# Optimization experiments

Measured on AMD Instinct MI355X. Metric: run time of the kernel, lower is better.

The kernel has to match this reference:

```python
import jax, jax.numpy as jnp
import numpy as np
import math

B, T, H, NB, D = 4, 4096, 16, 32, 1024
HID = 128

def setup_inputs() -> dict:
    key = jax.random.key(0)
    ks = jax.random.split(key, 12)
    s = lambda k, shape, fan: jax.random.normal(k, shape, jnp.float32) * (1.0 / np.sqrt(fan))
    return {
        "theta_path": jax.random.normal(ks[0], (B, T, H, NB), jnp.float32),
        "content_emb": jax.random.normal(ks[1], (B, T, D), jnp.float32),
        "mw1": s(ks[2], (D, HID), D), "mb1": jnp.zeros((HID,), jnp.float32),
        "mw2": s(ks[3], (HID, H * NB), HID), "mb2": jnp.zeros((H * NB,), jnp.float32),
        "gw1": s(ks[4], (D, HID), D), "gb1": jnp.zeros((HID,), jnp.float32),
        "gw2": s(ks[5], (HID, H * NB), HID), "gb2": jnp.zeros((H * NB,), jnp.float32),
        "log_Q": jnp.full((H, NB), -3.0, jnp.float32),
        "log_R": jnp.full((H, NB), 1.0, jnp.float32),
        "log_sigma0": jnp.zeros((H, NB), jnp.float32),
    }

def reference(theta_path, content_emb, mw1, mb1, mw2, mb2, gw1, gb1, gw2, gb2, log_Q, log_R, log_sigma0):
    b, t = theta_path.shape[:2]
    Q = jnp.exp(log_Q)          # (H, NB)
    R = jnp.exp(log_R)          # (H, NB)
    sigma0 = jnp.exp(log_sigma0)
    # measurement head and gate (exact GELU as in torch nn.GELU default)
    h1 = jax.nn.gelu(content_emb @ mw1 + mb1, approximate=False)
    z = jnp.pi * jnp.tanh((h1 @ mw2 + mb2).reshape(b, t, H, NB))
    h2 = jax.nn.gelu(content_emb @ gw1 + gb1, approximate=False)
    g = jax.nn.sigmoid((h2 @ gw2 + gb2).reshape(b, t, H, NB))
    # per-step increments: incs[0]=theta_path[0], incs[t]=theta_path[t]-theta_path[t-1]
    incs = jnp.concatenate([theta_path[:, :1], theta_path[:, 1:] - theta_path[:, :-1]], axis=1)

    def step(carry, xs):
        theta_hat, sigma = carry
        inc_t, z_t, g_t = xs                     # each (B, H, NB)
        theta_hat = theta_hat + inc_t
        sigma = sigma + Q
        diff = z_t - theta_hat
        innov = jnp.arctan2(jnp.sin(diff), jnp.cos(diff))
        R_eff = R / (g_t + 1e-4)
        K = sigma / (sigma + R_eff)
        theta_hat = theta_hat + K * innov
        sigma = (1.0 - K) * sigma
        return (theta_hat, sigma), (theta_hat, sigma)

    init = (jnp.zeros((b, H, NB), theta_path.dtype),
            jnp.broadcast_to(sigma0, (b, H, NB)))
    xs = (jnp.swapaxes(incs, 0, 1), jnp.swapaxes(z, 0, 1), jnp.swapaxes(g, 0, 1))
    _, (theta_seq, sigma_seq) = jax.lax.scan(step, init, xs)
    theta_hat_out = jnp.swapaxes(theta_seq, 0, 1)   # (B, T, H, NB)
    sigma_out = jnp.swapaxes(sigma_seq, 0, 1)
    return theta_hat_out, sigma_out, g
```

## Files before the change

kernel.cpp:

```cpp
#include <hip/hip_runtime.h>
#include <cstdint>
#include <cstddef>

typedef _Float16 half8  __attribute__((ext_vector_type(8)));
typedef float    f32x4  __attribute__((ext_vector_type(4)));

constexpr int Bc = 4, Tc = 4096, Hc = 16, NBc = 32, Dc = 1024, HIDc = 128;
constexpr int HN = Hc * NBc;
constexpr int BT = Bc * Tc;

__device__ inline void split8(const float* __restrict__ p,
                              _Float16* __restrict__ dh,
                              _Float16* __restrict__ dl) {
  float4 a = *reinterpret_cast<const float4*>(p);
  float4 b = *reinterpret_cast<const float4*>(p + 4);
  float v[8] = {a.x, a.y, a.z, a.w, b.x, b.y, b.z, b.w};
  half8 hi, lo;
#pragma unroll
  for (int j = 0; j < 8; j++) {
    _Float16 h = (_Float16)v[j];
    hi[j] = h;
    lo[j] = (_Float16)(v[j] - (float)h);
  }
  *reinterpret_cast<half8*>(dh) = hi;
  *reinterpret_cast<half8*>(dl) = lo;
}

__global__ __launch_bounds__(256) void k_split_w(
    const float* __restrict__ mw1, const float* __restrict__ gw1,
    const float* __restrict__ mw2, const float* __restrict__ gw2,
    _Float16* __restrict__ W1Thi, _Float16* __restrict__ W1Tlo,
    _Float16* __restrict__ W2Thi, _Float16* __restrict__ W2Tlo) {
  unsigned i = blockIdx.x * 256u + threadIdx.x;
  if (i < 262144u) {
    unsigned n = i >> 10, k = i & 1023u;
    float v = (n < 128u) ? mw1[k * 128u + n] : gw1[k * 128u + (n - 128u)];
    _Float16 h = (_Float16)v;
    W1Thi[i] = h;
    W1Tlo[i] = (_Float16)(v - (float)h);
  } else {
    unsigned j2 = i - 262144u;
    unsigned n = j2 >> 7, k = j2 & 127u;
    float v = (n < 512u) ? mw2[k * 512u + n] : gw2[k * 512u + (n - 512u)];
    _Float16 h = (_Float16)v;
    W2Thi[j2] = h;
    W2Tlo[j2] = (_Float16)(v - (float)h);
  }
}

__global__ __launch_bounds__(256) void k_gemm1(
    const float* __restrict__ X,
    const _Float16* __restrict__ Whi, const _Float16* __restrict__ Wlo,
    const float* __restrict__ mb1, const float* __restrict__ gb1,
    _Float16* __restrict__ Hhi, _Float16* __restrict__ Hlo) {
  __shared__ _Float16 sAh[128][40], sAl[128][40];
  __shared__ _Float16 sBh[64][40],  sBl[64][40];
  const int tid  = threadIdx.x;
  const int lane = tid & 63;
  const int w    = tid >> 6;
  const int wr   = w >> 1, wc = w & 1;
  const int rm   = blockIdx.x * 128;
  const int cn   = blockIdx.y * 64;
  const int lr   = lane & 15, kg = (lane >> 4) * 8;

  f32x4 acc[4][2] = {};

  for (int kt = 0; kt < 1024; kt += 32) {
#pragma unroll
    for (int j = 0; j < 2; j++) {
      int row = j * 64 + (tid >> 2);
      int k0  = (tid & 3) * 8;
      size_t g = (size_t)(rm + row) * 1024 + kt + k0;
      split8(X + g, &sAh[row][k0], &sAl[row][k0]);
    }
    {
      int n  = tid >> 2;
      int k0 = (tid & 3) * 8;
      size_t g = (size_t)(cn + n) * 1024 + kt + k0;
      *reinterpret_cast<uint4*>(&sBh[n][k0]) = *reinterpret_cast<const uint4*>(Whi + g);
      *reinterpret_cast<uint4*>(&sBl[n][k0]) = *reinterpret_cast<const uint4*>(Wlo + g);
    }
    __syncthreads();

    half8 ah[4], al[4], bh[2], bl[2];
#pragma unroll
    for (int m = 0; m < 4; m++) {
      ah[m] = *reinterpret_cast<const half8*>(&sAh[wr * 64 + m * 16 + lr][kg]);
      al[m] = *reinterpret_cast<const half8*>(&sAl[wr * 64 + m * 16 + lr][kg]);
    }
#pragma unroll
    for (int n = 0; n < 2; n++) {
      bh[n] = *reinterpret_cast<const half8*>(&sBh[wc * 32 + n * 16 + lr][kg]);
      bl[n] = *reinterpret_cast<const half8*>(&sBl[wc * 32 + n * 16 + lr][kg]);
    }
#pragma unroll
    for (int m = 0; m < 4; m++)
#pragma unroll
      for (int n = 0; n < 2; n++) {
        acc[m][n] = __builtin_amdgcn_mfma_f32_16x16x32_f16(ah[m], bh[n], acc[m][n], 0, 0, 0);
        acc[m][n] = __builtin_amdgcn_mfma_f32_16x16x32_f16(ah[m], bl[n], acc[m][n], 0, 0, 0);
        acc[m][n] = __builtin_amdgcn_mfma_f32_16x16x32_f16(al[m], bh[n], acc[m][n], 0, 0, 0);
      }
    __syncthreads();
  }

#pragma unroll
  for (int n = 0; n < 2; n++) {
    int colg = cn + wc * 32 + n * 16 + lr;
    float bias = (colg < 128) ? mb1[colg] : gb1[colg - 128];
#pragma unroll
    for (int m = 0; m < 4; m++) {
#pragma unroll
      for (int r = 0; r < 4; r++) {
        int rowg = rm + wr * 64 + m * 16 + (lane >> 4) * 4 + r;
        float v  = acc[m][n][r] + bias;
        float ge = 0.5f * v * (1.0f + erff(v * 0.70710678118654752f));
        _Float16 h = (_Float16)ge;
        Hhi[(size_t)rowg * 256 + colg] = h;
        Hlo[(size_t)rowg * 256 + colg] = (_Float16)(ge - (float)h);
      }
    }
  }
}

__global__ __launch_bounds__(256) void k_gemm2(
    const _Float16* __restrict__ Hhi, const _Float16* __restrict__ Hlo,
    const _Float16* __restrict__ Whi, const _Float16* __restrict__ Wlo,
    const float* __restrict__ mb2, const float* __restrict__ gb2,
    float* __restrict__ zbuf, float* __restrict__ gout) {
  __shared__ _Float16 sAh[128][40], sAl[128][40];
  __shared__ _Float16 sBh[64][40],  sBl[64][40];
  const int tid  = threadIdx.x;
  const int lane = tid & 63;
  const int w    = tid >> 6;
  const int wr   = w >> 1, wc = w & 1;
  const int rm   = blockIdx.x * 128;
  const int cn   = blockIdx.y * 64;
  const int khead = (cn < 512) ? 0 : 128;
  const int lr   = lane & 15, kg = (lane >> 4) * 8;

  f32x4 acc[4][2] = {};

  for (int kt = 0; kt < 128; kt += 32) {
#pragma unroll
    for (int j = 0; j < 2; j++) {
      int row = j * 64 + (tid >> 2);
      int k0  = (tid & 3) * 8;
      size_t g = (size_t)(rm + row) * 256 + khead + kt + k0;
      *reinterpret_cast<uint4*>(&sAh[row][k0]) = *reinterpret_cast<const uint4*>(Hhi + g);
      *reinterpret_cast<uint4*>(&sAl[row][k0]) = *reinterpret_cast<const uint4*>(Hlo + g);
    }
    {
      int n  = tid >> 2;
      int k0 = (tid & 3) * 8;
      size_t g = (size_t)(cn + n) * 128 + kt + k0;
      *reinterpret_cast<uint4*>(&sBh[n][k0]) = *reinterpret_cast<const uint4*>(Whi + g);
      *reinterpret_cast<uint4*>(&sBl[n][k0]) = *reinterpret_cast<const uint4*>(Wlo + g);
    }
    __syncthreads();

    half8 ah[4], al[4], bh[2], bl[2];
#pragma unroll
    for (int m = 0; m < 4; m++) {
      ah[m] = *reinterpret_cast<const half8*>(&sAh[wr * 64 + m * 16 + lr][kg]);
      al[m] = *reinterpret_cast<const half8*>(&sAl[wr * 64 + m * 16 + lr][kg]);
    }
#pragma unroll
    for (int n = 0; n < 2; n++) {
      bh[n] = *reinterpret_cast<const half8*>(&sBh[wc * 32 + n * 16 + lr][kg]);
      bl[n] = *reinterpret_cast<const half8*>(&sBl[wc * 32 + n * 16 + lr][kg]);
    }
#pragma unroll
    for (int m = 0; m < 4; m++)
#pragma unroll
      for (int n = 0; n < 2; n++) {
        acc[m][n] = __builtin_amdgcn_mfma_f32_16x16x32_f16(ah[m], bh[n], acc[m][n], 0, 0, 0);
        acc[m][n] = __builtin_amdgcn_mfma_f32_16x16x32_f16(ah[m], bl[n], acc[m][n], 0, 0, 0);
        acc[m][n] = __builtin_amdgcn_mfma_f32_16x16x32_f16(al[m], bh[n], acc[m][n], 0, 0, 0);
      }
    __syncthreads();
  }

  const float PI = 3.14159265358979323846f;
#pragma unroll
  for (int n = 0; n < 2; n++) {
    int colg = cn + wc * 32 + n * 16 + lr;
    bool isz = (colg < 512);
    float bias = isz ? mb2[colg] : gb2[colg - 512];
#pragma unroll
    for (int m = 0; m < 4; m++) {
#pragma unroll
      for (int r = 0; r < 4; r++) {
        int rowg = rm + wr * 64 + m * 16 + (lane >> 4) * 4 + r;
        float v  = acc[m][n][r] + bias;
        if (isz) {
          zbuf[(size_t)rowg * 512 + colg] = PI * tanhf(v);
        } else {
          gout[(size_t)rowg * 512 + (colg - 512)] = 1.0f / (1.0f + expf(-v));
        }
      }
    }
  }
}

__global__ __launch_bounds__(64) void k_mob1(
    const float* __restrict__ g, const float* __restrict__ logQ,
    const float* __restrict__ logR, float* __restrict__ Mbuf) {
  const int c  = blockIdx.x * 64 + threadIdx.x;
  const int ts = blockIdx.y;
  const int b  = c >> 9, hn = c & 511;
  const float Q = expf(logQ[hn]);
  const float R = expf(logR[hn]);
  const unsigned base = (unsigned)b * (unsigned)(Tc * HN) + (unsigned)(ts * 64) * (unsigned)HN + (unsigned)hn;

  float ma = 1.f, mb = 0.f, mc = 0.f, md = 1.f;
  float gv[32];
#pragma unroll 1
  for (int ph = 0; ph < 2; ph++) {
#pragma unroll
    for (int j = 0; j < 32; j++) gv[j] = g[base + (unsigned)(ph * 32 + j) * 512u];
#pragma unroll
    for (int j = 0; j < 32; j++) {
      float re = R * __builtin_amdgcn_rcpf(gv[j] + 1e-4f);
      float t1 = __builtin_fmaf(Q, mc, ma);
      float t2 = __builtin_fmaf(Q, md, mb);
      ma = re * t1;
      mb = re * t2;
      mc = __builtin_fmaf(re, mc, t1);
      md = __builtin_fmaf(re, md, t2);
      if ((j & 3) == 3) {
        float r = __builtin_amdgcn_rcpf(md);
        ma *= r; mb *= r; mc *= r; md *= r;
      }
    }
  }
  f32x4 M; M[0] = ma; M[1] = mb; M[2] = mc; M[3] = md;
  reinterpret_cast<f32x4*>(Mbuf)[ts * 2048 + c] = M;
}

__global__ __launch_bounds__(64) void k_mob2(
    const float* __restrict__ Mbuf, const float* __restrict__ logS0,
    float* __restrict__ sstart) {
  const int c  = blockIdx.x * 64 + threadIdx.x;
  const int hn = c & 511;
  float s = expf(logS0[hn]);
  const f32x4* M4 = reinterpret_cast<const f32x4*>(Mbuf);
  f32x4 ring[8];
#pragma unroll
  for (int i = 0; i < 8; i++) ring[i] = M4[i * 2048 + c];
#pragma unroll
  for (int ts = 0; ts < 64; ts++) {
    sstart[ts * 2048 + c] = s;
    f32x4 M = ring[ts & 7];
    if (ts + 8 < 64) ring[ts & 7] = M4[(ts + 8) * 2048 + c];
    s = (M[0] * s + M[1]) / (M[2] * s + M[3]);
  }
}

__global__ __launch_bounds__(64) void k_mob3(
    const float* __restrict__ g, const float* __restrict__ logQ,
    const float* __restrict__ logR, const float* __restrict__ sstart,
    float* __restrict__ Kbuf, float* __restrict__ osig) {
  const int c  = blockIdx.x * 64 + threadIdx.x;
  const int ts = blockIdx.y;
  const int b  = c >> 9, hn = c & 511;
  const float Q = expf(logQ[hn]);
  const float R = expf(logR[hn]);
  const unsigned base = (unsigned)b * (unsigned)(Tc * HN) + (unsigned)(ts * 64) * (unsigned)HN + (unsigned)hn;

  float s = sstart[ts * 2048 + c];
  float gv[32];
#pragma unroll 1
  for (int ph = 0; ph < 2; ph++) {
#pragma unroll
    for (int j = 0; j < 32; j++) gv[j] = g[base + (unsigned)(ph * 32 + j) * 512u];
#pragma unroll
    for (int j = 0; j < 32; j++) {
      const unsigned idx = base + (unsigned)(ph * 32 + j) * 512u;
      float re = R * __builtin_amdgcn_rcpf(gv[j] + 1e-4f);
      float sp = s + Q;
      float K  = sp * __builtin_amdgcn_rcpf(sp + re);
      s = K * re;
      Kbuf[idx] = K;
      osig[idx] = s;
    }
  }
}

__global__ __launch_bounds__(448) void k_scan_theta(
    const float* __restrict__ tp, const float* __restrict__ zarr,
    const float* __restrict__ Karr, float* __restrict__ oth) {
  __shared__ float4 ibuf[2][3][16][64];
  __shared__ float4 obuf[2][16][64];
  const int tid  = threadIdx.x;
  const int lane = tid & 63;
  const int wv   = tid >> 6;
  const int c    = blockIdx.x * 64 + lane;
  const int b    = c >> 9;
  const int hn   = c & 511;
  const unsigned base = (unsigned)b * (unsigned)(Tc * HN) + (unsigned)hn;

  constexpr float INV2PI = 0.15915494309189535f;
  constexpr float TWOPI  = 6.283185307179586f;

  const int s = (wv - 1) >> 1;
  const int h = (wv - 1) & 1;
  const float* src = (s == 0) ? tp : (s == 1) ? zarr : Karr;

  float theta = 0.f, tprev = 0.f;

  auto load_chunk = [&](int k) {
    float r[32];
    const unsigned tb0 = (unsigned)(k * 64 + h * 32);
#pragma unroll
    for (int j = 0; j < 32; j++) r[j] = src[base + (tb0 + (unsigned)j) * 512u];
#pragma unroll
    for (int jj = 0; jj < 8; jj++) {
      float4 v; v.x = r[4*jj]; v.y = r[4*jj+1]; v.z = r[4*jj+2]; v.w = r[4*jj+3];
      ibuf[k & 1][s][h * 8 + jj][lane] = v;
    }
  };

  if (wv >= 1) load_chunk(0);
  __syncthreads();

#pragma unroll 1
  for (int k = 0; k <= 64; k++) {
    if (wv == 0) {
      if (k < 64) {
        const int db = k & 1;
        float4 A[3][4], B[3][4];

        auto LOADQ = [&](float4 (&dst)[3][4], int q) {
#pragma unroll
          for (int m2 = 0; m2 < 4; m2++)
#pragma unroll
            for (int st = 0; st < 3; st++)
              dst[st][m2] = ibuf[db][st][q * 4 + m2][lane];
        };
        auto COMPQ = [&](float4 (&sq)[3][4], int q) {
#pragma unroll
          for (int m2 = 0; m2 < 4; m2++) {
            float4 t4 = sq[0][m2], z4 = sq[1][m2], K4 = sq[2][m2];
            float4 th;
#pragma unroll
            for (int j = 0; j < 4; j++) {
              float tpv = (j == 0) ? t4.x : (j == 1) ? t4.y : (j == 2) ? t4.z : t4.w;
              float zv  = (j == 0) ? z4.x : (j == 1) ? z4.y : (j == 2) ? z4.z : z4.w;
              float Kv  = (j == 0) ? K4.x : (j == 1) ? K4.y : (j == 2) ? K4.z : K4.w;
              float inc = tpv - tprev; tprev = tpv;
              float thp = theta + inc;
              float d   = zv - thp;
              float nr  = rintf(d * INV2PI);
              float innov = __builtin_fmaf(-TWOPI, nr, d);
              theta = __builtin_fmaf(Kv, innov, thp);
              if (j == 0) th.x = theta; else if (j == 1) th.y = theta;
              else if (j == 2) th.z = theta; else th.w = theta;
            }
            obuf[db][q * 4 + m2][lane] = th;
          }
        };

        LOADQ(A, 0);
        LOADQ(B, 1); COMPQ(A, 0);
        LOADQ(A, 2); COMPQ(B, 1);
        LOADQ(B, 3); COMPQ(A, 2);
        COMPQ(B, 3);
      }
    } else {
      if (k >= 1) {
        const unsigned tbase = (unsigned)((k - 1) * 64);
        const int fdb = (k - 1) & 1;
#pragma unroll
        for (int i = 0; i < 3; i++) {
          int tb = (wv - 1) + 6 * i;
          if (tb < 16) {
            float4 v = obuf[fdb][tb][lane];
            oth[base + (tbase + (unsigned)(4 * tb)    ) * 512u] = v.x;
            oth[base + (tbase + (unsigned)(4 * tb + 1)) * 512u] = v.y;
            oth[base + (tbase + (unsigned)(4 * tb + 2)) * 512u] = v.z;
            oth[base + (tbase + (unsigned)(4 * tb + 3)) * 512u] = v.w;
          }
        }
      }
      if (k + 1 < 64) load_chunk(k + 1);
    }
    __syncthreads();
  }
}

extern "C" void kernel_launch(void* const* d_in, const int* in_sizes, int n_in,
                              void* d_out, int out_size, void* d_ws, size_t ws_size,
                              hipStream_t stream) {
  const float* theta_path = (const float*)d_in[0];
  const float* X     = (const float*)d_in[1];
  const float* mw1   = (const float*)d_in[2];
  const float* mb1   = (const float*)d_in[3];
  const float* mw2   = (const float*)d_in[4];
  const float* mb2   = (const float*)d_in[5];
  const float* gw1   = (const float*)d_in[6];
  const float* gb1   = (const float*)d_in[7];
  const float* gw2   = (const float*)d_in[8];
  const float* gb2   = (const float*)d_in[9];
  const float* logQ  = (const float*)d_in[10];
  const float* logR  = (const float*)d_in[11];
  const float* logS0 = (const float*)d_in[12];

  const size_t NOUT = (size_t)BT * HN;
  float* out_theta = (float*)d_out;
  float* out_sigma = out_theta + NOUT;
  float* out_g     = out_theta + 2 * NOUT;

  float* Kbuf = out_theta;

  char* ws = (char*)d_ws;
  _Float16* W1Thi = (_Float16*)(ws);
  _Float16* W1Tlo = (_Float16*)(ws + (512u << 10));
  _Float16* W2Thi = (_Float16*)(ws + (1024u << 10));
  _Float16* W2Tlo = (_Float16*)(ws + (1280u << 10));
  _Float16* Hhi   = (_Float16*)(ws + (1536u << 10));
  _Float16* Hlo   = (_Float16*)(ws + (1536u << 10) + (8u << 20));
  float*    zbuf  = (float*)  (ws + (1536u << 10) + (16u << 20));
  float*    Mbuf  = (float*)  (ws + (1536u << 10) + (48u << 20));
  float*    sst   = (float*)  (ws + (1536u << 10) + (50u << 20));

  k_split_w<<<1536, 256, 0, stream>>>(mw1, gw1, mw2, gw2, W1Thi, W1Tlo, W2Thi, W2Tlo);
  k_gemm1<<<dim3(128, 4), 256, 0, stream>>>(X, W1Thi, W1Tlo, mb1, gb1, Hhi, Hlo);
  k_gemm2<<<dim3(128, 16), 256, 0, stream>>>(Hhi, Hlo, W2Thi, W2Tlo, mb2, gb2, zbuf, out_g);
  k_mob1<<<dim3(32, 64), 64, 0, stream>>>(out_g, logQ, logR, Mbuf);
  k_mob2<<<32, 64, 0, stream>>>(Mbuf, logS0, sst);
  k_mob3<<<dim3(32, 64), 64, 0, stream>>>(out_g, logQ, logR, sst, Kbuf, out_sigma);
  k_scan_theta<<<32, 448, 0, stream>>>(theta_path, zbuf, Kbuf, out_theta);
}
```

Baseline: 192.1 us.

## Fuse Kalman gain/sigma recurrence into theta scan kernel loader warps

Removes the separate k_mob3 kernel that wrote K to a scratch buffer, and has the two loader warps in k_scan_theta that previously streamed K instead recompute the sigma/K recurrence from g and the chunk start sigma. The second-half warp redoes the first 32 steps to obtain its starting state. This drops a full K write plus re-read and one launch, at the cost of more serial work inside the single 32-block scan kernel, which may become the critical path.

```diff
diff --git a/kernel.cpp b/kernel.cpp
--- a/kernel.cpp
+++ b/kernel.cpp
@@ -257,39 +257,11 @@
   }
 }
 
-__global__ __launch_bounds__(64) void k_mob3(
-    const float* __restrict__ g, const float* __restrict__ logQ,
-    const float* __restrict__ logR, const float* __restrict__ sstart,
-    float* __restrict__ Kbuf, float* __restrict__ osig) {
-  const int c  = blockIdx.x * 64 + threadIdx.x;
-  const int ts = blockIdx.y;
-  const int b  = c >> 9, hn = c & 511;
-  const float Q = expf(logQ[hn]);
-  const float R = expf(logR[hn]);
-  const unsigned base = (unsigned)b * (unsigned)(Tc * HN) + (unsigned)(ts * 64) * (unsigned)HN + (unsigned)hn;
-
-  float s = sstart[ts * 2048 + c];
-  float gv[32];
-#pragma unroll 1
-  for (int ph = 0; ph < 2; ph++) {
-#pragma unroll
-    for (int j = 0; j < 32; j++) gv[j] = g[base + (unsigned)(ph * 32 + j) * 512u];
-#pragma unroll
-    for (int j = 0; j < 32; j++) {
-      const unsigned idx = base + (unsigned)(ph * 32 + j) * 512u;
-      float re = R * __builtin_amdgcn_rcpf(gv[j] + 1e-4f);
-      float sp = s + Q;
-      float K  = sp * __builtin_amdgcn_rcpf(sp + re);
-      s = K * re;
-      Kbuf[idx] = K;
-      osig[idx] = s;
-    }
-  }
-}
-
 __global__ __launch_bounds__(448) void k_scan_theta(
     const float* __restrict__ tp, const float* __restrict__ zarr,
-    const float* __restrict__ Karr, float* __restrict__ oth) {
+    const float* __restrict__ garr, const float* __restrict__ logQ,
+    const float* __restrict__ logR, const float* __restrict__ sstart,
+    float* __restrict__ oth, float* __restrict__ osig) {
   __shared__ float4 ibuf[2][3][16][64];
   __shared__ float4 obuf[2][16][64];
   const int tid  = threadIdx.x;
@@ -305,11 +277,13 @@
 
   const int s = (wv - 1) >> 1;
   const int h = (wv - 1) & 1;
-  const float* src = (s == 0) ? tp : (s == 1) ? zarr : Karr;
+  const float Q = expf(logQ[hn]);
+  const float R = expf(logR[hn]);
 
   float theta = 0.f, tprev = 0.f;
 
   auto load_chunk = [&](int k) {
+    const float* src = (s == 0) ? tp : zarr;
     float r[32];
     const unsigned tb0 = (unsigned)(k * 64 + h * 32);
 #pragma unroll
@@ -321,7 +295,58 @@
     }
   };
 
-  if (wv >= 1) load_chunk(0);
+  auto gwork = [&](int k) {
+    float s_run = sstart[k * 2048 + c];
+    const unsigned tb0 = (unsigned)(k * 64);
+    if (h == 0) {
+      float gv[32], Ks[32];
+#pragma unroll
+      for (int j = 0; j < 32; j++) gv[j] = garr[base + (tb0 + (unsigned)j) * 512u];
+#pragma unroll
+      for (int j = 0; j < 32; j++) {
+        float re = R * __builtin_amdgcn_rcpf(gv[j] + 1e-4f);
+        float sp = s_run + Q;
+        float K  = sp * __builtin_amdgcn_rcpf(sp + re);
+        s_run = K * re;
+        Ks[j] = K;
+        osig[base + (tb0 + (unsigned)j) * 512u] = s_run;
+      }
+#pragma unroll
+      for (int jj = 0; jj < 8; jj++) {
+        float4 v; v.x = Ks[4*jj]; v.y = Ks[4*jj+1]; v.z = Ks[4*jj+2]; v.w = Ks[4*jj+3];
+        ibuf[k & 1][2][jj][lane] = v;
+      }
+    } else {
+      float gv[64], Ks[32];
+#pragma unroll
+      for (int j = 0; j < 64; j++) gv[j] = garr[base + (tb0 + (unsigned)j) * 512u];
+#pragma unroll
+      for (int j = 0; j < 32; j++) {
+        float re = R * __builtin_amdgcn_rcpf(gv[j] + 1e-4f);
+        float sp = s_run + Q;
+        float K  = sp * __builtin_amdgcn_rcpf(sp + re);
+        s_run = K * re;
+      }
+#pragma unroll
+      for (int j = 32; j < 64; j++) {
+        float re = R * __builtin_amdgcn_rcpf(gv[j] + 1e-4f);
+        float sp = s_run + Q;
+        float K  = sp * __builtin_amdgcn_rcpf(sp + re);
+        s_run = K * re;
+        Ks[j - 32] = K;
+        osig[base + (tb0 + (unsigned)j) * 512u] = s_run;
+      }
+#pragma unroll
+      for (int jj = 0; jj < 8; jj++) {
+        float4 v; v.x = Ks[4*jj]; v.y = Ks[4*jj+1]; v.z = Ks[4*jj+2]; v.w = Ks[4*jj+3];
+        ibuf[k & 1][2][8 + jj][lane] = v;
+      }
+    }
+  };
+
+  if (wv >= 1) {
+    if (s == 2) gwork(0); else load_chunk(0);
+  }
   __syncthreads();
 
 #pragma unroll 1
@@ -383,7 +408,9 @@
           }
         }
       }
-      if (k + 1 < 64) load_chunk(k + 1);
+      if (k + 1 < 64) {
+        if (s == 2) gwork(k + 1); else load_chunk(k + 1);
+      }
     }
     __syncthreads();
   }
@@ -411,8 +438,6 @@
   float* out_sigma = out_theta + NOUT;
   float* out_g     = out_theta + 2 * NOUT;
 
-  float* Kbuf = out_theta;
-
   char* ws = (char*)d_ws;
   _Float16* W1Thi = (_Float16*)(ws);
   _Float16* W1Tlo = (_Float16*)(ws + (512u << 10));
@@ -429,6 +454,6 @@
   k_gemm2<<<dim3(128, 16), 256, 0, stream>>>(Hhi, Hlo, W2Thi, W2Tlo, mb2, gb2, zbuf, out_g);
   k_mob1<<<dim3(32, 64), 64, 0, stream>>>(out_g, logQ, logR, Mbuf);
   k_mob2<<<32, 64, 0, stream>>>(Mbuf, logS0, sst);
-  k_mob3<<<dim3(32, 64), 64, 0, stream>>>(out_g, logQ, logR, sst, Kbuf, out_sigma);
-  k_scan_theta<<<32, 448, 0, stream>>>(theta_path, zbuf, Kbuf, out_theta);
-}
+  k_scan_theta<<<32, 448, 0, stream>>>(theta_path, zbuf, out_g, logQ, logR, sst,
+                                       out_theta, out_sigma);
+}
```

Result: slower. 261.7 us (+36.2%).
